# Optimization experiments

Measured on AMD Instinct MI355X. Metric: run time of the kernel, lower is better.

The kernel has to match this reference:

```python
import jax, jax.numpy as jnp
import numpy as np

N_NODES = 50000
N_EDGES = 800000
NFEAT, NHID, NCLASS = 512, 128, 64


def setup_inputs() -> dict:
    key = jax.random.key(0)
    ks = jax.random.split(key, 8)
    rows = jnp.sort(jax.random.randint(ks[1], (N_EDGES,), 0, N_NODES, dtype=jnp.int64 if jax.config.jax_enable_x64 else jnp.int32))
    cols = jax.random.randint(ks[2], (N_EDGES,), 0, N_NODES, dtype=rows.dtype)
    return {
        "x": jax.random.normal(ks[0], (N_NODES, NFEAT), dtype=jnp.float32),
        "rows": rows,
        "cols": cols,
        "vals": jax.random.uniform(ks[3], (N_EDGES,), dtype=jnp.float32),
        "W1": jax.random.normal(ks[4], (NFEAT, NHID), dtype=jnp.float32) * (1.0 / np.sqrt(NHID)),
        "b1": jax.random.normal(ks[5], (NHID,), dtype=jnp.float32) * 0.01,
        "W2": jax.random.normal(ks[6], (NHID, NCLASS), dtype=jnp.float32) * (1.0 / np.sqrt(NCLASS)),
        "b2": jax.random.normal(ks[7], (NCLASS,), dtype=jnp.float32) * 0.01,
    }


def _spmm(rows, cols, vals, h, num_nodes):
    # A @ h where A is sparse (num_nodes x num_nodes) given as COO edges.
    # Equivalent math to the custom flexspmm segmented SpMM kernel.
    msgs = vals[:, None] * h[cols]              # [E, d]
    return jax.ops.segment_sum(msgs, rows, num_segments=num_nodes)


def reference(x, rows, cols, vals, W1, b1, W2, b2):
    n = x.shape[0]
    # Layer 1: A @ (X W1) + b1   (GraphConvolution)
    h = x @ W1
    h = _spmm(rows, cols, vals, h, n) + b1
    h = jax.nn.relu(h)
    # dropout: eval mode -> identity
    # Layer 2: (A @ h) W2 + b2   (GraphConvolution2)
    h = _spmm(rows, cols, vals, h, n)
    logits = h @ W2 + b2
    return jax.nn.log_softmax(logits, axis=1)
```

## Files before the change

### kernel.cpp

```cpp
#include <hip/hip_runtime.h>
#include <hip/hip_bf16.h>
#include <math.h>


#define N_NODES 50000
#define N_EDGES 800000
#define NFEAT   512
#define NHID    128
#define NCLASS  64

typedef short  short8  __attribute__((ext_vector_type(8)));
typedef unsigned short ushort8 __attribute__((ext_vector_type(8)));
typedef float  f32x4   __attribute__((ext_vector_type(4)));

static __device__ __forceinline__ unsigned short f2bf(float f) {
    unsigned int b = __builtin_bit_cast(unsigned int, f);
    return (unsigned short)((b + 0x7FFFu + ((b >> 16) & 1u)) >> 16);
}
static __device__ __forceinline__ float bf2f(unsigned short u) {
    return __builtin_bit_cast(float, ((unsigned int)u) << 16);
}

__global__ __launch_bounds__(256) void prep_kernel(
        const float* __restrict__ W1, const float* __restrict__ W2,
        const int* __restrict__ rows,
        unsigned short* __restrict__ W1T, unsigned short* __restrict__ W2T,
        int* __restrict__ row_ptr) {
    const int tid = blockIdx.x * 256 + threadIdx.x;
    const int T   = gridDim.x * 256;
    for (int e = tid; e < N_EDGES; e += T) {
        const int re = rows[e];
        if (e == 0) {
            for (int r = 0; r <= re; ++r) row_ptr[r] = 0;
        } else {
            const int rp = rows[e - 1];
            for (int r = rp + 1; r <= re; ++r) row_ptr[r] = e;
        }
        if (e == N_EDGES - 1) {
            for (int r = re + 1; r <= N_NODES; ++r) row_ptr[r] = N_EDGES;
        }
    }
    for (int i = tid; i < NHID * NFEAT; i += T) {
        const int n = i >> 9, k = i & 511;
        W1T[i] = f2bf(W1[(size_t)k * NHID + n]);
    }
    for (int i = tid; i < NCLASS * NHID; i += T) {
        const int n = i >> 7, k = i & 127;
        W2T[i] = f2bf(W2[(size_t)k * NCLASS + n]);
    }
}

__global__ __launch_bounds__(256) void gemm1_kernel(
        const float* __restrict__ x, const unsigned short* __restrict__ W1T,
        unsigned short* __restrict__ h1b, int M) {
    __shared__ unsigned short sA[64 * 64];
    __shared__ unsigned short sB[128 * 64];

    const int tid  = threadIdx.x;
    const int lane = tid & 63;
    const int wid  = tid >> 6;
    const int wr   = wid >> 1, wc = wid & 1;
    const int row0 = blockIdx.x * 64;

    f32x4 acc[2][4];
    #pragma unroll
    for (int i = 0; i < 2; ++i)
        #pragma unroll
        for (int j = 0; j < 4; ++j)
            acc[i][j] = (f32x4){0.f, 0.f, 0.f, 0.f};

    const int arow = tid >> 2;
    const int akc  = (tid & 3) * 16;
    const int bcol = tid >> 1;
    const int bkh  = (tid & 1) * 32;

    for (int kt = 0; kt < NFEAT; kt += 64) {
        {
            float v[16];
            const float* src = x + (size_t)(row0 + arow) * NFEAT + kt + akc;
            if (row0 + arow < M) {
                #pragma unroll
                for (int i = 0; i < 4; ++i)
                    *(float4*)&v[i * 4] = *(const float4*)(src + i * 4);
            } else {
                #pragma unroll
                for (int i = 0; i < 16; ++i) v[i] = 0.f;
            }
            #pragma unroll
            for (int i2 = 0; i2 < 2; ++i2) {
                ushort8 w;
                #pragma unroll
                for (int q = 0; q < 8; ++q) w[q] = f2bf(v[i2 * 8 + q]);
                const int gran = ((akc >> 3) + i2) ^ (arow & 7);
                *(ushort8*)((char*)sA + arow * 128 + gran * 16) = w;
            }
        }
        {
            const unsigned short* srcb = W1T + (size_t)bcol * NFEAT + kt + bkh;
            #pragma unroll
            for (int i = 0; i < 4; ++i) {
                ushort8 w = *(const ushort8*)(srcb + i * 8);
                const int gran = ((bkh >> 3) + i) ^ (bcol & 7);
                *(ushort8*)((char*)sB + bcol * 128 + gran * 16) = w;
            }
        }
        __syncthreads();

        #pragma unroll
        for (int ks = 0; ks < 2; ++ks) {
            short8 af[2], bfr[4];
            #pragma unroll
            for (int i = 0; i < 2; ++i) {
                const int ar = wr * 32 + i * 16 + (lane & 15);
                const int gran = (ks * 4 + (lane >> 4)) ^ (ar & 7);
                af[i] = *(const short8*)((const char*)sA + ar * 128 + gran * 16);
            }
            #pragma unroll
            for (int j = 0; j < 4; ++j) {
                const int br = wc * 64 + j * 16 + (lane & 15);
                const int gran = (ks * 4 + (lane >> 4)) ^ (br & 7);
                bfr[j] = *(const short8*)((const char*)sB + br * 128 + gran * 16);
            }
            #pragma unroll
            for (int i = 0; i < 2; ++i)
                #pragma unroll
                for (int j = 0; j < 4; ++j)
                    acc[i][j] = __builtin_amdgcn_mfma_f32_16x16x32_bf16(
                        af[i], bfr[j], acc[i][j], 0, 0, 0);
        }
        __syncthreads();
    }

    const int cr = (lane >> 4) * 4;
    const int cc = lane & 15;
    #pragma unroll
    for (int i = 0; i < 2; ++i)
        #pragma unroll
        for (int j = 0; j < 4; ++j)
            #pragma unroll
            for (int reg = 0; reg < 4; ++reg) {
                const int row = row0 + wr * 32 + i * 16 + cr + reg;
                const int col = wc * 64 + j * 16 + cc;
                if (row < M)
                    h1b[(size_t)row * NHID + col] = f2bf(acc[i][j][reg]);
            }
}

__global__ __launch_bounds__(256) void spmm1_kernel(
        const int* __restrict__ row_ptr, const int* __restrict__ cols,
        const float* __restrict__ vals, const unsigned short* __restrict__ h1b,
        const float* __restrict__ b1, unsigned short* __restrict__ h2b) {
    const int lane = threadIdx.x & 63;
    const int g = lane >> 4;
    const int s = lane & 15;
    const int r = (blockIdx.x * 256 + threadIdx.x) >> 6;
    if (r >= N_NODES) return;

    const int lo = row_ptr[r], hi = row_ptr[r + 1];
    float acc[8];
    #pragma unroll
    for (int q = 0; q < 8; ++q) acc[q] = 0.f;

    int e = lo;
    for (; e + 8 <= hi; e += 8) {
        const int e0 = e + g, e1 = e + 4 + g;
        const float v0 = __builtin_nontemporal_load(vals + e0);
        const float v1 = __builtin_nontemporal_load(vals + e1);
        const int   c0 = __builtin_nontemporal_load(cols + e0);
        const int   c1 = __builtin_nontemporal_load(cols + e1);
        const ushort8 p0 = *(const ushort8*)(h1b + (size_t)c0 * NHID + s * 8);
        const ushort8 p1 = *(const ushort8*)(h1b + (size_t)c1 * NHID + s * 8);
        #pragma unroll
        for (int q = 0; q < 8; ++q) {
            acc[q] = fmaf(v0, bf2f(p0[q]), acc[q]);
            acc[q] = fmaf(v1, bf2f(p1[q]), acc[q]);
        }
    }
    for (; e < hi; e += 4) {
        const int ee = e + g;
        ushort8 p = {0, 0, 0, 0, 0, 0, 0, 0};
        float v = 0.f;
        if (ee < hi) {
            v = vals[ee];
            const int c = cols[ee];
            p = *(const ushort8*)(h1b + (size_t)c * NHID + s * 8);
        }
        #pragma unroll
        for (int q = 0; q < 8; ++q)
            acc[q] = fmaf(v, bf2f(p[q]), acc[q]);
    }

    #pragma unroll
    for (int q = 0; q < 8; ++q) {
        acc[q] += __shfl_xor(acc[q], 16, 64);
        acc[q] += __shfl_xor(acc[q], 32, 64);
    }

    if (g == 0) {
        float bv[8];
        *(float4*)&bv[0] = *(const float4*)(b1 + s * 8);
        *(float4*)&bv[4] = *(const float4*)(b1 + s * 8 + 4);
        ushort8 o;
        #pragma unroll
        for (int q = 0; q < 8; ++q) {
            float a = acc[q] + bv[q];
            o[q] = f2bf(a > 0.f ? a : 0.f);
        }
        *(ushort8*)(h2b + (size_t)r * NHID + s * 8) = o;
    }
}

__global__ __launch_bounds__(256) void gemm2_kernel(
        const unsigned short* __restrict__ h2b,
        const unsigned short* __restrict__ W2T,
        unsigned short* __restrict__ tb, int nwaves) {
    const int lane = threadIdx.x & 63;
    const int wave = (blockIdx.x * 256 + threadIdx.x) >> 6;
    const int l15 = lane & 15, lg = lane >> 4;

    short8 Bf[4][4];
    #pragma unroll
    for (int ks = 0; ks < 4; ++ks)
        #pragma unroll
        for (int ct = 0; ct < 4; ++ct)
            Bf[ks][ct] = *(const short8*)(W2T + (size_t)(ct * 16 + l15) * NHID + ks * 32 + lg * 8);

    const int ntiles = N_NODES / 16;
    for (int t = wave; t < ntiles; t += nwaves) {
        const int r0 = t * 16;
        f32x4 acc[4];
        #pragma unroll
        for (int ct = 0; ct < 4; ++ct) acc[ct] = (f32x4){0.f, 0.f, 0.f, 0.f};
        #pragma unroll
        for (int ks = 0; ks < 4; ++ks) {
            short8 af = *(const short8*)(h2b + (size_t)(r0 + l15) * NHID + ks * 32 + lg * 8);
            #pragma unroll
            for (int ct = 0; ct < 4; ++ct)
                acc[ct] = __builtin_amdgcn_mfma_f32_16x16x32_bf16(af, Bf[ks][ct], acc[ct], 0, 0, 0);
        }
        #pragma unroll
        for (int ct = 0; ct < 4; ++ct)
            #pragma unroll
            for (int reg = 0; reg < 4; ++reg)
                tb[(size_t)(r0 + lg * 4 + reg) * NCLASS + ct * 16 + l15] = f2bf(acc[ct][reg]);
    }
}

__global__ __launch_bounds__(256) void spmm2_lsm_kernel(
        const int* __restrict__ row_ptr, const int* __restrict__ cols,
        const float* __restrict__ vals, const unsigned short* __restrict__ tb,
        const float* __restrict__ b2, float* __restrict__ out) {
    const int lane = threadIdx.x & 63;
    const int g = lane >> 3;
    const int s = lane & 7;
    const int r = (blockIdx.x * 256 + threadIdx.x) >> 6;
    if (r >= N_NODES) return;

    const int lo = row_ptr[r], hi = row_ptr[r + 1];
    float acc[8];
    #pragma unroll
    for (int q = 0; q < 8; ++q) acc[q] = 0.f;

    int e = lo;
    for (; e + 16 <= hi; e += 16) {
        const int e0 = e + g, e1 = e + 8 + g;
        const float v0 = __builtin_nontemporal_load(vals + e0);
        const float v1 = __builtin_nontemporal_load(vals + e1);
        const int   c0 = __builtin_nontemporal_load(cols + e0);
        const int   c1 = __builtin_nontemporal_load(cols + e1);
        const ushort8 p0 = *(const ushort8*)(tb + (size_t)c0 * NCLASS + s * 8);
        const ushort8 p1 = *(const ushort8*)(tb + (size_t)c1 * NCLASS + s * 8);
        #pragma unroll
        for (int q = 0; q < 8; ++q) {
            acc[q] = fmaf(v0, bf2f(p0[q]), acc[q]);
            acc[q] = fmaf(v1, bf2f(p1[q]), acc[q]);
        }
    }
    for (; e < hi; e += 8) {
        const int ee = e + g;
        ushort8 p = {0, 0, 0, 0, 0, 0, 0, 0};
        float v = 0.f;
        if (ee < hi) {
            v = vals[ee];
            const int c = cols[ee];
            p = *(const ushort8*)(tb + (size_t)c * NCLASS + s * 8);
        }
        #pragma unroll
        for (int q = 0; q < 8; ++q)
            acc[q] = fmaf(v, bf2f(p[q]), acc[q]);
    }

    #pragma unroll
    for (int q = 0; q < 8; ++q) {
        acc[q] += __shfl_xor(acc[q], 8, 64);
        acc[q] += __shfl_xor(acc[q], 16, 64);
        acc[q] += __shfl_xor(acc[q], 32, 64);
    }

    float l[8];
    {
        float bv[8];
        *(float4*)&bv[0] = *(const float4*)(b2 + s * 8);
        *(float4*)&bv[4] = *(const float4*)(b2 + s * 8 + 4);
        #pragma unroll
        for (int q = 0; q < 8; ++q) l[q] = acc[q] + bv[q];
    }

    float m = l[0];
    #pragma unroll
    for (int q = 1; q < 8; ++q) m = fmaxf(m, l[q]);
    m = fmaxf(m, __shfl_xor(m, 1, 64));
    m = fmaxf(m, __shfl_xor(m, 2, 64));
    m = fmaxf(m, __shfl_xor(m, 4, 64));

    float sum = 0.f;
    #pragma unroll
    for (int q = 0; q < 8; ++q) sum += __expf(l[q] - m);
    sum += __shfl_xor(sum, 1, 64);
    sum += __shfl_xor(sum, 2, 64);
    sum += __shfl_xor(sum, 4, 64);
    const float ls = __logf(sum);

    if (lane < 8) {
        float4 o0, o1;
        o0.x = l[0] - m - ls; o0.y = l[1] - m - ls;
        o0.z = l[2] - m - ls; o0.w = l[3] - m - ls;
        o1.x = l[4] - m - ls; o1.y = l[5] - m - ls;
        o1.z = l[6] - m - ls; o1.w = l[7] - m - ls;
        *(float4*)(out + (size_t)r * NCLASS + s * 8)     = o0;
        *(float4*)(out + (size_t)r * NCLASS + s * 8 + 4) = o1;
    }
}

extern "C" void kernel_launch(void* const* d_in, const int* in_sizes, int n_in,
                              void* d_out, int out_size, void* d_ws, size_t ws_size,
                              hipStream_t stream) {
    const float* x    = (const float*)d_in[0];
    const int*   rows = (const int*)  d_in[1];
    const int*   cols = (const int*)  d_in[2];
    const float* vals = (const float*)d_in[3];
    const float* W1   = (const float*)d_in[4];
    const float* b1   = (const float*)d_in[5];
    const float* W2   = (const float*)d_in[6];
    const float* b2   = (const float*)d_in[7];
    float* out = (float*)d_out;

    unsigned short* h1b = (unsigned short*)d_ws;
    unsigned short* h2b = h1b + (size_t)N_NODES * NHID;
    unsigned short* tb  = h2b + (size_t)N_NODES * NHID;
    unsigned short* W1T = tb  + (size_t)N_NODES * NCLASS;
    unsigned short* W2T = W1T + (size_t)NHID * NFEAT;
    int* row_ptr = (int*)(W2T + (size_t)NCLASS * NHID);

    const int M = N_NODES;

    prep_kernel<<<2048, 256, 0, stream>>>(W1, W2, rows, W1T, W2T, row_ptr);
    gemm1_kernel<<<(M + 63) / 64, 256, 0, stream>>>(x, W1T, h1b, M);
    spmm1_kernel<<<(M * 64 + 255) / 256, 256, 0, stream>>>(row_ptr, cols, vals, h1b, b1, h2b);
    gemm2_kernel<<<782, 256, 0, stream>>>(h2b, W2T, tb, 782 * 4);
    spmm2_lsm_kernel<<<(M * 64 + 255) / 256, 256, 0, stream>>>(row_ptr, cols, vals, tb, b2, out);
}
```

Before: 256.9 us.

## Prefetch GEMM tiles into registers and batch SpMM edge loads via wave shuffles

The dense X·W1 GEMM now loads the next K-tile of X and W1T into registers while MFMAs run on the current shared-memory tile, hiding global load latency behind compute. This costs extra registers. Both SpMM kernels now load up to 64 edge indices and values coalesced, one per lane, and broadcast them with wave shuffles. They then issue four independent gathers per iteration instead of two, aiming for more memory-level parallelism and fewer scattered index loads. Rows with few edges (about 16 on average) may waste some lanes on masked-out work.

```diff
diff --git a/kernel.cpp b/kernel.cpp
--- a/kernel.cpp
+++ b/kernel.cpp
@@ -73,38 +73,52 @@
     const int akc  = (tid & 3) * 16;
     const int bcol = tid >> 1;
     const int bkh  = (tid & 1) * 32;
+    const bool arow_ok = (row0 + arow < M);
+    const float* asrc = x + (size_t)(row0 + arow) * NFEAT + akc;
+    const unsigned short* bsrc = W1T + (size_t)bcol * NFEAT + bkh;
+
+    float   va[16];
+    ushort8 vb[4];
+
+    if (arow_ok) {
+        #pragma unroll
+        for (int i = 0; i < 4; ++i)
+            *(float4*)&va[i * 4] = *(const float4*)(asrc + i * 4);
+    } else {
+        #pragma unroll
+        for (int i = 0; i < 16; ++i) va[i] = 0.f;
+    }
+    #pragma unroll
+    for (int i = 0; i < 4; ++i) vb[i] = *(const ushort8*)(bsrc + i * 8);
 
     for (int kt = 0; kt < NFEAT; kt += 64) {
-        {
-            float v[16];
-            const float* src = x + (size_t)(row0 + arow) * NFEAT + kt + akc;
-            if (row0 + arow < M) {
+        __syncthreads();
+        #pragma unroll
+        for (int i2 = 0; i2 < 2; ++i2) {
+            ushort8 w;
+            #pragma unroll
+            for (int q = 0; q < 8; ++q) w[q] = f2bf(va[i2 * 8 + q]);
+            const int gran = ((akc >> 3) + i2) ^ (arow & 7);
+            *(ushort8*)((char*)sA + arow * 128 + gran * 16) = w;
+        }
+        #pragma unroll
+        for (int i = 0; i < 4; ++i) {
+            const int gran = ((bkh >> 3) + i) ^ (bcol & 7);
+            *(ushort8*)((char*)sB + bcol * 128 + gran * 16) = vb[i];
+        }
+        __syncthreads();
+
+        const int ktn = kt + 64;
+        if (ktn < NFEAT) {
+            if (arow_ok) {
                 #pragma unroll
                 for (int i = 0; i < 4; ++i)
-                    *(float4*)&v[i * 4] = *(const float4*)(src + i * 4);
-            } else {
-                #pragma unroll
-                for (int i = 0; i < 16; ++i) v[i] = 0.f;
-            }
-            #pragma unroll
-            for (int i2 = 0; i2 < 2; ++i2) {
-                ushort8 w;
-                #pragma unroll
-                for (int q = 0; q < 8; ++q) w[q] = f2bf(v[i2 * 8 + q]);
-                const int gran = ((akc >> 3) + i2) ^ (arow & 7);
-                *(ushort8*)((char*)sA + arow * 128 + gran * 16) = w;
-            }
-        }
-        {
-            const unsigned short* srcb = W1T + (size_t)bcol * NFEAT + kt + bkh;
-            #pragma unroll
-            for (int i = 0; i < 4; ++i) {
-                ushort8 w = *(const ushort8*)(srcb + i * 8);
-                const int gran = ((bkh >> 3) + i) ^ (bcol & 7);
-                *(ushort8*)((char*)sB + bcol * 128 + gran * 16) = w;
-            }
-        }
-        __syncthreads();
+                    *(float4*)&va[i * 4] = *(const float4*)(asrc + ktn + i * 4);
+            }
+            #pragma unroll
+            for (int i = 0; i < 4; ++i)
+                vb[i] = *(const ushort8*)(bsrc + ktn + i * 8);
+        }
 
         #pragma unroll
         for (int ks = 0; ks < 2; ++ks) {
@@ -128,7 +142,6 @@
                     acc[i][j] = __builtin_amdgcn_mfma_f32_16x16x32_bf16(
                         af[i], bfr[j], acc[i][j], 0, 0, 0);
         }
-        __syncthreads();
     }
 
     const int cr = (lane >> 4) * 4;
@@ -157,37 +170,36 @@
     if (r >= N_NODES) return;
 
     const int lo = row_ptr[r], hi = row_ptr[r + 1];
+    const int n = hi - lo;
+
     float acc[8];
     #pragma unroll
     for (int q = 0; q < 8; ++q) acc[q] = 0.f;
 
-    int e = lo;
-    for (; e + 8 <= hi; e += 8) {
-        const int e0 = e + g, e1 = e + 4 + g;
-        const float v0 = __builtin_nontemporal_load(vals + e0);
-        const float v1 = __builtin_nontemporal_load(vals + e1);
-        const int   c0 = __builtin_nontemporal_load(cols + e0);
-        const int   c1 = __builtin_nontemporal_load(cols + e1);
-        const ushort8 p0 = *(const ushort8*)(h1b + (size_t)c0 * NHID + s * 8);
-        const ushort8 p1 = *(const ushort8*)(h1b + (size_t)c1 * NHID + s * 8);
-        #pragma unroll
-        for (int q = 0; q < 8; ++q) {
-            acc[q] = fmaf(v0, bf2f(p0[q]), acc[q]);
-            acc[q] = fmaf(v1, bf2f(p1[q]), acc[q]);
-        }
-    }
-    for (; e < hi; e += 4) {
-        const int ee = e + g;
-        ushort8 p = {0, 0, 0, 0, 0, 0, 0, 0};
-        float v = 0.f;
-        if (ee < hi) {
-            v = vals[ee];
-            const int c = cols[ee];
-            p = *(const ushort8*)(h1b + (size_t)c * NHID + s * 8);
-        }
-        #pragma unroll
-        for (int q = 0; q < 8; ++q)
-            acc[q] = fmaf(v, bf2f(p[q]), acc[q]);
+    for (int base = 0; base < n; base += 64) {
+        const int idxl = lo + base + lane;
+        const float vl = (idxl < hi) ? vals[idxl] : 0.f;
+        const int   cl = (idxl < hi) ? cols[idxl] : 0;
+        const int cnt = min(64, n - base);
+        for (int i0 = 0; i0 < cnt; i0 += 16) {
+            float v[4]; int c[4];
+            #pragma unroll
+            for (int u = 0; u < 4; ++u) {
+                const int idx = i0 + 4 * u + g;
+                v[u] = __shfl(vl, idx, 64);
+                c[u] = __shfl(cl, idx, 64);
+                if (idx >= cnt) { v[u] = 0.f; c[u] = 0; }
+            }
+            ushort8 p[4];
+            #pragma unroll
+            for (int u = 0; u < 4; ++u)
+                p[u] = *(const ushort8*)(h1b + (size_t)c[u] * NHID + s * 8);
+            #pragma unroll
+            for (int u = 0; u < 4; ++u)
+                #pragma unroll
+                for (int q = 0; q < 8; ++q)
+                    acc[q] = fmaf(v[u], bf2f(p[u][q]), acc[q]);
+        }
     }
 
     #pragma unroll
@@ -257,37 +269,36 @@
     if (r >= N_NODES) return;
 
     const int lo = row_ptr[r], hi = row_ptr[r + 1];
+    const int n = hi - lo;
+
     float acc[8];
     #pragma unroll
     for (int q = 0; q < 8; ++q) acc[q] = 0.f;
 
-    int e = lo;
-    for (; e + 16 <= hi; e += 16) {
-        const int e0 = e + g, e1 = e + 8 + g;
-        const float v0 = __builtin_nontemporal_load(vals + e0);
-        const float v1 = __builtin_nontemporal_load(vals + e1);
-        const int   c0 = __builtin_nontemporal_load(cols + e0);
-        const int   c1 = __builtin_nontemporal_load(cols + e1);
-        const ushort8 p0 = *(const ushort8*)(tb + (size_t)c0 * NCLASS + s * 8);
-        const ushort8 p1 = *(const ushort8*)(tb + (size_t)c1 * NCLASS + s * 8);
-        #pragma unroll
-        for (int q = 0; q < 8; ++q) {
-            acc[q] = fmaf(v0, bf2f(p0[q]), acc[q]);
-            acc[q] = fmaf(v1, bf2f(p1[q]), acc[q]);
-        }
-    }
-    for (; e < hi; e += 8) {
-        const int ee = e + g;
-        ushort8 p = {0, 0, 0, 0, 0, 0, 0, 0};
-        float v = 0.f;
-        if (ee < hi) {
-            v = vals[ee];
-            const int c = cols[ee];
-            p = *(const ushort8*)(tb + (size_t)c * NCLASS + s * 8);
-        }
-        #pragma unroll
-        for (int q = 0; q < 8; ++q)
-            acc[q] = fmaf(v, bf2f(p[q]), acc[q]);
+    for (int base = 0; base < n; base += 64) {
+        const int idxl = lo + base + lane;
+        const float vl = (idxl < hi) ? vals[idxl] : 0.f;
+        const int   cl = (idxl < hi) ? cols[idxl] : 0;
+        const int cnt = min(64, n - base);
+        for (int i0 = 0; i0 < cnt; i0 += 32) {
+            float v[4]; int c[4];
+            #pragma unroll
+            for (int u = 0; u < 4; ++u) {
+                const int idx = i0 + 8 * u + g;
+                v[u] = __shfl(vl, idx, 64);
+                c[u] = __shfl(cl, idx, 64);
+                if (idx >= cnt) { v[u] = 0.f; c[u] = 0; }
+            }
+            ushort8 p[4];
+            #pragma unroll
+            for (int u = 0; u < 4; ++u)
+                p[u] = *(const ushort8*)(tb + (size_t)c[u] * NCLASS + s * 8);
+            #pragma unroll
+            for (int u = 0; u < 4; ++u)
+                #pragma unroll
+                for (int q = 0; q < 8; ++q)
+                    acc[q] = fmaf(v[u], bf2f(p[u][q]), acc[q]);
+        }
     }
 
     #pragma unroll
```

After: 246.9 us. -3.9%, faster.
